# Kernel tuning notes

Measured on AMD Instinct MI355X. Metric: run time of the kernel, lower is better.

## Reference

```python
import jax, jax.numpy as jnp
import numpy as np

N_NODES = 100000
N_EDGES = 1000000
D = 128          # input_dim == hidden_dim (required: h = zeros_like(nh) accumulates src_nf)
OUT = 128
NUM_TYPES = 5


def setup_inputs() -> dict:
    key = jax.random.key(0)
    ks = jax.random.split(key, 7)
    nh = jax.random.normal(ks[0], (N_NODES, D), dtype=jnp.float32)
    edge_y = jax.random.randint(ks[1], (N_EDGES,), 0, NUM_TYPES, dtype=jnp.int64)
    edge_index = jax.random.randint(ks[2], (2, N_EDGES), 0, N_NODES, dtype=jnp.int64)
    # nn.Linear weights, scaled for numerical sanity
    W_nf = jax.random.normal(ks[3], (D, D), dtype=jnp.float32) * 0.08
    W_attn = jax.random.normal(ks[4], (1, 2 * D), dtype=jnp.float32) * 0.08
    W_out = jax.random.normal(ks[5], (OUT, 2 * D), dtype=jnp.float32) * 0.08
    b_out = jax.random.normal(ks[6], (OUT,), dtype=jnp.float32) * 0.01
    return {"nh": nh, "edge_y": edge_y, "edge_index": edge_index,
            "W_nf": W_nf, "W_attn": W_attn, "W_out": W_out, "b_out": b_out}


def reference(nh, edge_y, edge_index, W_nf, W_attn, W_out, b_out):
    n = nh.shape[0]
    src, dst = edge_index[0], edge_index[1]

    # nf_lin applied once per node, then gathered per edge (same math as
    # self.nf_lin(nh[src]) since Linear is per-row)
    nfl = nh @ W_nf.T                                  # [N, D]
    src_nf = nfl[src]                                  # [E, D]
    dst_nf = nfl[dst]                                  # [E, D]

    # attn(cat([src_nf, dst_nf])) == src_nf @ a_src + dst_nf @ a_dst
    a_src, a_dst = W_attn[0, :D], W_attn[0, D:]
    ef = src_nf @ a_src + dst_nf @ a_dst               # [E]
    ef = jnp.where(ef >= 0, ef, 0.2 * ef)              # LeakyReLU(0.2)

    # scatter_softmax per (edge_type, dst) group: the per-type loop with
    # scatter_softmax over dst is exactly a segment softmax over composite
    # segments seg = dst*5 + type; the summed per-type scatter_adds equal
    # one segment_sum over dst.
    seg = dst * NUM_TYPES + edge_y                     # [E]
    num_seg = n * NUM_TYPES
    m = jax.ops.segment_max(ef, seg, num_segments=num_seg)
    ex = jnp.exp(ef - m[seg])
    denom = jax.ops.segment_sum(ex, seg, num_segments=num_seg)
    alpha = ex / denom[seg]                            # [E]

    h = jax.ops.segment_sum(alpha[:, None] * src_nf, dst, num_segments=n)  # [N, D]

    nf = jnp.concatenate([nh, h], axis=-1) @ W_out.T + b_out
    return jax.nn.relu(nf)
```

## Files before the change

### kernel.cpp

```cpp
#include <hip/hip_runtime.h>

#define NTYPES 5
#define EPB 4096
#define BKSH 7
#define BKDST 128
#define SUBD 32
#define CAP 1024

typedef _Float16 half8 __attribute__((ext_vector_type(8)));
typedef _Float16 half4v __attribute__((ext_vector_type(4)));
typedef float float4v __attribute__((ext_vector_type(4)));

__device__ __forceinline__ void stage_f32(
    _Float16* lds, const float* __restrict__ g, int rows, int stride4, int off4,
    int grow0, int nmax, int t)
{
  const float4* g4 = (const float4*)g;
  for (int i = t; i < rows * 32; i += 256) {
    int row = i >> 5, q = i & 31;
    float4 v = make_float4(0.f, 0.f, 0.f, 0.f);
    int gr = grow0 + row;
    if (gr < nmax) v = g4[(size_t)gr * stride4 + off4 + q];
    half4v hv = { (_Float16)v.x, (_Float16)v.y, (_Float16)v.z, (_Float16)v.w };
    int byte = row * 256 + ((q * 8) ^ ((row & 7) << 4));
    *(half4v*)((char*)lds + byte) = hv;
  }
}

__device__ __forceinline__ half8 frag_ld(const _Float16* lds, int row, int khw) {
  int byte = row * 256 + ((khw * 2) ^ ((row & 7) << 4));
  return *(const half8*)((const char*)lds + byte);
}

__device__ __forceinline__ half8 cvt8(float4 v0, float4 v1) {
  half8 a;
  a[0] = (_Float16)v0.x; a[1] = (_Float16)v0.y; a[2] = (_Float16)v0.z; a[3] = (_Float16)v0.w;
  a[4] = (_Float16)v1.x; a[5] = (_Float16)v1.y; a[6] = (_Float16)v1.z; a[7] = (_Float16)v1.w;
  return a;
}

__global__ __launch_bounds__(256) void k_gemm0(
    const float* __restrict__ nh, const float* __restrict__ Wnf,
    const float* __restrict__ Wattn,
    float* __restrict__ s_src, float* __restrict__ s_dst,
    _Float16* __restrict__ nfl, _Float16* __restrict__ nh16, int n)
{
  __shared__ _Float16 wh[128 * 128];
  const int t = threadIdx.x, lane = t & 63, wv = t >> 6;
  const int r16 = lane & 15, g = lane >> 4;
  stage_f32(wh, Wnf, 128, 32, 0, 0, 1 << 30, t);
  float asrc[8], adst[8];
  #pragma unroll
  for (int nf = 0; nf < 8; ++nf) {
    asrc[nf] = Wattn[nf * 16 + r16];
    adst[nf] = Wattn[128 + nf * 16 + r16];
  }
  __syncthreads();
  const int nchunk = (n + 63) >> 6;
  for (int c = blockIdx.x; c < nchunk; c += gridDim.x) {
    const int base = c << 6;
    const int arow = base + wv * 16 + r16;
    const bool ok = arow < n;
    const float4* nh4 = (const float4*)(nh + (size_t)arow * 128);
    const float4 z = make_float4(0.f, 0.f, 0.f, 0.f);
    float4 av[8];
    #pragma unroll
    for (int s = 0; s < 4; ++s) {
      av[2 * s]     = ok ? nh4[s * 8 + g * 2]     : z;
      av[2 * s + 1] = ok ? nh4[s * 8 + g * 2 + 1] : z;
    }
    float4v acc[8];
    #pragma unroll
    for (int nf = 0; nf < 8; ++nf) acc[nf] = (float4v){0.f, 0.f, 0.f, 0.f};
    #pragma unroll
    for (int s = 0; s < 4; ++s) {
      half8 a = cvt8(av[2 * s], av[2 * s + 1]);
      if (ok) *(half8*)(nh16 + (size_t)arow * 128 + s * 32 + g * 8) = a;
      #pragma unroll
      for (int nf = 0; nf < 8; ++nf)
        acc[nf] = __builtin_amdgcn_mfma_f32_16x16x32_f16(a, frag_ld(wh, nf * 16 + r16, s * 32 + g * 8), acc[nf], 0, 0, 0);
    }
    #pragma unroll
    for (int rr = 0; rr < 4; ++rr) {
      int node = base + wv * 16 + g * 4 + rr;
      if (node >= n) continue;
      size_t ro = (size_t)node * 128;
      #pragma unroll
      for (int nf = 0; nf < 8; ++nf) nfl[ro + nf * 16 + r16] = (_Float16)acc[nf][rr];
    }
    float ss[4] = {0.f, 0.f, 0.f, 0.f}, sd[4] = {0.f, 0.f, 0.f, 0.f};
    #pragma unroll
    for (int nf = 0; nf < 8; ++nf)
      #pragma unroll
      for (int rr = 0; rr < 4; ++rr) {
        ss[rr] = fmaf(acc[nf][rr], asrc[nf], ss[rr]);
        sd[rr] = fmaf(acc[nf][rr], adst[nf], sd[rr]);
      }
    #pragma unroll
    for (int m = 1; m <= 8; m <<= 1)
      #pragma unroll
      for (int rr = 0; rr < 4; ++rr) {
        ss[rr] += __shfl_xor(ss[rr], m);
        sd[rr] += __shfl_xor(sd[rr], m);
      }
    if (r16 == 0) {
      #pragma unroll
      for (int rr = 0; rr < 4; ++rr) {
        int node = base + wv * 16 + g * 4 + rr;
        if (node < n) { s_src[node] = ss[rr]; s_dst[node] = sd[rr]; }
      }
    }
  }
}

__global__ __launch_bounds__(256) void k_hist(
    const int* __restrict__ dsts, int* __restrict__ cnt, int e, int nbk, int nblk)
{
  __shared__ int hist[1024];
  const int t = threadIdx.x, b = blockIdx.x;
  for (int k = t; k < nbk; k += 256) hist[k] = 0;
  __syncthreads();
  const int i0 = b * EPB;
  const int iend = min(i0 + EPB, e);
  for (int i = i0 + t; i < iend; i += 256)
    atomicAdd(&hist[dsts[i] >> BKSH], 1);
  __syncthreads();
  for (int k = t; k < nbk; k += 256) cnt[k * nblk + b] = hist[k];
}

__global__ __launch_bounds__(256) void k_scan1(
    const int* __restrict__ deg, int* __restrict__ base, int* __restrict__ bsum, int n)
{
  __shared__ int ws[4];
  int t = threadIdx.x;
  int g0 = blockIdx.x * 1024 + t * 4;
  int4 v = make_int4(0, 0, 0, 0);
  if (g0 + 3 < n) v = *(const int4*)(deg + g0);
  else {
    if (g0     < n) v.x = deg[g0];
    if (g0 + 1 < n) v.y = deg[g0 + 1];
    if (g0 + 2 < n) v.z = deg[g0 + 2];
    if (g0 + 3 < n) v.w = deg[g0 + 3];
  }
  int s = v.x + v.y + v.z + v.w;
  int inc = s;
  #pragma unroll
  for (int d = 1; d < 64; d <<= 1) {
    int o = __shfl_up(inc, d);
    if ((t & 63) >= d) inc += o;
  }
  int wid = t >> 6;
  if ((t & 63) == 63) ws[wid] = inc;
  __syncthreads();
  int woff = 0;
  for (int w = 0; w < wid; ++w) woff += ws[w];
  int exc = woff + inc - s;
  if (g0 + 3 < n) {
    *(int4*)(base + g0) = make_int4(exc, exc + v.x, exc + v.x + v.y, exc + v.x + v.y + v.z);
  } else {
    if (g0     < n) base[g0]     = exc;
    if (g0 + 1 < n) base[g0 + 1] = exc + v.x;
    if (g0 + 2 < n) base[g0 + 2] = exc + v.x + v.y;
  }
  if (t == 255) bsum[blockIdx.x] = woff + inc;
}

__global__ __launch_bounds__(256) void k_scan2(
    const int* __restrict__ bsum, int* __restrict__ boff, int nb)
{
  __shared__ int ws[4];
  int t = threadIdx.x;
  int x = t < nb ? bsum[t] : 0;
  int inc = x;
  #pragma unroll
  for (int d = 1; d < 64; d <<= 1) {
    int o = __shfl_up(inc, d);
    if ((t & 63) >= d) inc += o;
  }
  int wid = t >> 6;
  if ((t & 63) == 63) ws[wid] = inc;
  __syncthreads();
  int woff = 0;
  for (int w = 0; w < wid; ++w) woff += ws[w];
  if (t < nb) boff[t] = woff + inc - x;
}

__global__ __launch_bounds__(256) void k_scan3(
    int* __restrict__ base, const int* __restrict__ boff, int n)
{
  int i = blockIdx.x * 256 + threadIdx.x;
  if (i < n) base[i] += boff[i >> 10];
}

__global__ __launch_bounds__(256) void k_scatter2(
    const int* __restrict__ ei, const int* __restrict__ ey,
    const int* __restrict__ cnt_s, unsigned* __restrict__ rec,
    int e, int nbk, int nblk)
{
  __shared__ int cur[1024];
  const int t = threadIdx.x, b = blockIdx.x;
  for (int k = t; k < nbk; k += 256) cur[k] = cnt_s[k * nblk + b];
  __syncthreads();
  const int i0 = b * EPB;
  const int iend = min(i0 + EPB, e);
  for (int i = i0 + t; i < iend; i += 256) {
    int s = ei[i], d = ei[e + i], ty = ey[i];
    int pos = atomicAdd(&cur[d >> BKSH], 1);
    rec[pos] = (unsigned)s | ((unsigned)ty << 17) | ((unsigned)(d & (BKDST - 1)) << 20);
  }
}

__global__ __launch_bounds__(256) void k_agg2(
    const unsigned* __restrict__ rec, const int* __restrict__ cnt_s,
    const float* __restrict__ s_src, const float* __restrict__ s_dst,
    const _Float16* __restrict__ nfl, _Float16* __restrict__ h,
    int n, int e, int nbk, int nblk)
{
  __shared__ unsigned ord[CAP];
  __shared__ float efl[CAP];
  __shared__ int dcnt[SUBD];
  __shared__ int dbase[SUBD + 1];
  __shared__ float sdl[SUBD];
  const int t = threadIdx.x;
  const int sb = blockIdx.x;
  const int d0 = sb << 5;
  const int ndst = min(SUBD, n - d0);
  const int k = sb >> 2;
  const int sub = sb & 3;
  const int bs = cnt_s[k * nblk];
  const int be = (k + 1 < nbk) ? cnt_s[(k + 1) * nblk] : e;
  const int cnt = be - bs;
  if (t < SUBD) {
    dcnt[t] = 0;
    if (t < ndst) sdl[t] = s_dst[d0 + t];
  }
  __syncthreads();
  const int g = t >> 4, l = t & 15;

  for (int i = t; i < cnt; i += 256) {
    int dl = (rec[bs + i] >> 20) & 127;
    if ((dl >> 5) == sub) atomicAdd(&dcnt[dl & 31], 1);
  }
  __syncthreads();
  if (t < SUBD) {
    int v = dcnt[t];
    int inc = v;
    #pragma unroll
    for (int dd = 1; dd < SUBD; dd <<= 1) {
      int o = __shfl_up(inc, dd);
      if (t >= dd) inc += o;
    }
    dbase[t] = inc - v;
    dcnt[t]  = inc - v;
    if (t == SUBD - 1) dbase[SUBD] = inc;
  }
  __syncthreads();
  const int total = dbase[SUBD];

  if (total <= CAP) {
    for (int i = t; i < cnt; i += 256) {
      unsigned p = rec[bs + i];
      int dl = (p >> 20) & 127;
      if ((dl >> 5) == sub) {
        int pos = atomicAdd(&dcnt[dl & 31], 1);
        ord[pos] = p;
      }
    }
    __syncthreads();
    for (int i = t; i < total; i += 256) {
      unsigned p = ord[i];
      float ef = s_src[p & 0x1FFFF] + sdl[(p >> 20) & 31];
      efl[i] = ef >= 0.f ? ef : 0.2f * ef;
    }
    __syncthreads();
    for (int di = g; di < ndst; di += 16) {
      int s0 = dbase[di], deg = dbase[di + 1] - s0;
      float acc[8] = {0.f, 0.f, 0.f, 0.f, 0.f, 0.f, 0.f, 0.f};
      if (deg > 0) {
        float mx[NTYPES];
        #pragma unroll
        for (int tt = 0; tt < NTYPES; ++tt) mx[tt] = -1e30f;
        for (int j0 = 0; j0 < deg; j0 += 16) {
          int jj = j0 + l;
          bool ok = jj < deg;
          float ef = ok ? efl[s0 + jj] : -1e30f;
          int ty = ok ? (int)((ord[s0 + jj] >> 17) & 7) : 7;
          #pragma unroll
          for (int tt = 0; tt < NTYPES; ++tt) {
            float v = (ty == tt) ? ef : -1e30f;
            v = fmaxf(v, __shfl_xor(v, 1)); v = fmaxf(v, __shfl_xor(v, 2));
            v = fmaxf(v, __shfl_xor(v, 4)); v = fmaxf(v, __shfl_xor(v, 8));
            mx[tt] = fmaxf(mx[tt], v);
          }
        }
        float sm[NTYPES];
        #pragma unroll
        for (int tt = 0; tt < NTYPES; ++tt) sm[tt] = 0.f;
        for (int j0 = 0; j0 < deg; j0 += 16) {
          int jj = j0 + l;
          bool ok = jj < deg;
          int ty = ok ? (int)((ord[s0 + jj] >> 17) & 7) : 7;
          float ex = ok ? __expf(efl[s0 + jj] - mx[ty]) : 0.f;
          if (ok) efl[s0 + jj] = ex;
          #pragma unroll
          for (int tt = 0; tt < NTYPES; ++tt) {
            float v = (ty == tt) ? ex : 0.f;
            v += __shfl_xor(v, 1); v += __shfl_xor(v, 2);
            v += __shfl_xor(v, 4); v += __shfl_xor(v, 8);
            sm[tt] += v;
          }
        }
        float rsm[NTYPES];
        #pragma unroll
        for (int tt = 0; tt < NTYPES; ++tt) rsm[tt] = sm[tt] > 0.f ? 1.f / sm[tt] : 0.f;
        int j = 0;
        for (; j + 4 <= deg; j += 4) {
          unsigned p0 = ord[s0 + j],     p1 = ord[s0 + j + 1];
          unsigned p2 = ord[s0 + j + 2], p3 = ord[s0 + j + 3];
          float a0 = efl[s0 + j]     * rsm[(p0 >> 17) & 7];
          float a1 = efl[s0 + j + 1] * rsm[(p1 >> 17) & 7];
          float a2 = efl[s0 + j + 2] * rsm[(p2 >> 17) & 7];
          float a3 = efl[s0 + j + 3] * rsm[(p3 >> 17) & 7];
          half8 x0 = *(const half8*)(nfl + (size_t)(p0 & 0x1FFFF) * 128 + l * 8);
          half8 x1 = *(const half8*)(nfl + (size_t)(p1 & 0x1FFFF) * 128 + l * 8);
          half8 x2 = *(const half8*)(nfl + (size_t)(p2 & 0x1FFFF) * 128 + l * 8);
          half8 x3 = *(const half8*)(nfl + (size_t)(p3 & 0x1FFFF) * 128 + l * 8);
          #pragma unroll
          for (int kk = 0; kk < 8; ++kk) acc[kk] = fmaf(a0, (float)x0[kk], acc[kk]);
          #pragma unroll
          for (int kk = 0; kk < 8; ++kk) acc[kk] = fmaf(a1, (float)x1[kk], acc[kk]);
          #pragma unroll
          for (int kk = 0; kk < 8; ++kk) acc[kk] = fmaf(a2, (float)x2[kk], acc[kk]);
          #pragma unroll
          for (int kk = 0; kk < 8; ++kk) acc[kk] = fmaf(a3, (float)x3[kk], acc[kk]);
        }
        for (; j < deg; ++j) {
          unsigned p0 = ord[s0 + j];
          float a0 = efl[s0 + j] * rsm[(p0 >> 17) & 7];
          half8 x0 = *(const half8*)(nfl + (size_t)(p0 & 0x1FFFF) * 128 + l * 8);
          #pragma unroll
          for (int kk = 0; kk < 8; ++kk) acc[kk] = fmaf(a0, (float)x0[kk], acc[kk]);
        }
      }
      half8 hv;
      #pragma unroll
      for (int kk = 0; kk < 8; ++kk) hv[kk] = (_Float16)acc[kk];
      *(half8*)(h + (size_t)(d0 + di) * 128 + l * 8) = hv;
    }
  } else {
    const int gb = (t & 63) & 48;
    for (int di = g; di < ndst; di += 16) {
      const int want = sub * SUBD + di;
      float mx[NTYPES], sm[NTYPES];
      #pragma unroll
      for (int tt = 0; tt < NTYPES; ++tt) { mx[tt] = -1e30f; sm[tt] = 0.f; }
      for (int j0 = 0; j0 < cnt; j0 += 16) {
        int jj = j0 + l;
        unsigned p = (jj < cnt) ? rec[bs + jj] : 0xFFFFFFFFu;
        bool mine = (p != 0xFFFFFFFFu) && (int)((p >> 20) & 127) == want;
        float ef = -1e30f; int ty = 7;
        if (mine) {
          ef = s_src[p & 0x1FFFF] + sdl[di];
          ef = ef >= 0.f ? ef : 0.2f * ef;
          ty = (p >> 17) & 7;
        }
        #pragma unroll
        for (int tt = 0; tt < NTYPES; ++tt) {
          float v = (mine && ty == tt) ? ef : -1e30f;
          v = fmaxf(v, __shfl_xor(v, 1)); v = fmaxf(v, __shfl_xor(v, 2));
          v = fmaxf(v, __shfl_xor(v, 4)); v = fmaxf(v, __shfl_xor(v, 8));
          mx[tt] = fmaxf(mx[tt], v);
        }
      }
      for (int j0 = 0; j0 < cnt; j0 += 16) {
        int jj = j0 + l;
        unsigned p = (jj < cnt) ? rec[bs + jj] : 0xFFFFFFFFu;
        bool mine = (p != 0xFFFFFFFFu) && (int)((p >> 20) & 127) == want;
        float ex = 0.f; int ty = 7;
        if (mine) {
          float ef = s_src[p & 0x1FFFF] + sdl[di];
          ef = ef >= 0.f ? ef : 0.2f * ef;
          ty = (p >> 17) & 7;
          ex = __expf(ef - mx[ty]);
        }
        #pragma unroll
        for (int tt = 0; tt < NTYPES; ++tt) {
          float v = (ty == tt) ? ex : 0.f;
          v += __shfl_xor(v, 1); v += __shfl_xor(v, 2);
          v += __shfl_xor(v, 4); v += __shfl_xor(v, 8);
          sm[tt] += v;
        }
      }
      float rsm[NTYPES];
      #pragma unroll
      for (int tt = 0; tt < NTYPES; ++tt) rsm[tt] = sm[tt] > 0.f ? 1.f / sm[tt] : 0.f;
      float acc[8] = {0.f, 0.f, 0.f, 0.f, 0.f, 0.f, 0.f, 0.f};
      for (int j0 = 0; j0 < cnt; j0 += 16) {
        int jj = j0 + l;
        unsigned p = (jj < cnt) ? rec[bs + jj] : 0xFFFFFFFFu;
        bool mine = (p != 0xFFFFFFFFu) && (int)((p >> 20) & 127) == want;
        float al = 0.f;
        if (mine) {
          float ef = s_src[p & 0x1FFFF] + sdl[di];
          ef = ef >= 0.f ? ef : 0.2f * ef;
          int ty = (p >> 17) & 7;
          al = __expf(ef - mx[ty]) * rsm[ty];
        }
        unsigned pv = mine ? p : 0xFFFFFFFFu;
        for (int jj2 = 0; jj2 < 16; ++jj2) {
          unsigned pp = __shfl(pv, gb + jj2);
          float aa = __shfl(al, gb + jj2);
          if (pp != 0xFFFFFFFFu) {
            half8 x = *(const half8*)(nfl + (size_t)(pp & 0x1FFFF) * 128 + l * 8);
            #pragma unroll
            for (int kk = 0; kk < 8; ++kk) acc[kk] = fmaf(aa, (float)x[kk], acc[kk]);
          }
        }
      }
      half8 hv;
      #pragma unroll
      for (int kk = 0; kk < 8; ++kk) hv[kk] = (_Float16)acc[kk];
      *(half8*)(h + (size_t)(d0 + di) * 128 + l * 8) = hv;
    }
  }
}

__global__ __launch_bounds__(256) void k_gemmO(
    const _Float16* __restrict__ nh16, const _Float16* __restrict__ hbuf,
    const float* __restrict__ Wout, const float* __restrict__ bias,
    float* __restrict__ out, int n)
{
  __shared__ _Float16 w1[64 * 128], w2[64 * 128];
  const int t = threadIdx.x, lane = t & 63, wv = t >> 6;
  const int r16 = lane & 15, g = lane >> 4;
  const int jhalf = blockIdx.x & 1;
  stage_f32(w1, Wout, 64, 64, 0,  jhalf * 64, 1 << 30, t);
  stage_f32(w2, Wout, 64, 64, 32, jhalf * 64, 1 << 30, t);
  float bv[4];
  #pragma unroll
  for (int nf = 0; nf < 4; ++nf) bv[nf] = bias[jhalf * 64 + nf * 16 + r16];
  __syncthreads();
  const int nchunk = (n + 63) >> 6;
  const int gstride = gridDim.x >> 1;
  int c = blockIdx.x >> 1;
  half8 c1[4], c2[4];
  if (c < nchunk) {
    int arow = (c << 6) + wv * 16 + r16;
    bool ok = arow < n;
    #pragma unroll
    for (int s = 0; s < 4; ++s) {
      c1[s] = ok ? *(const half8*)(nh16 + (size_t)arow * 128 + s * 32 + g * 8) : (half8){};
      c2[s] = ok ? *(const half8*)(hbuf + (size_t)arow * 128 + s * 32 + g * 8) : (half8){};
    }
  }
  for (; c < nchunk; c += gstride) {
    const int base = c << 6;
    int cn = c + gstride;
    half8 n1[4] = {}, n2[4] = {};
    if (cn < nchunk) {
      int arow = (cn << 6) + wv * 16 + r16;
      bool ok = arow < n;
      #pragma unroll
      for (int s = 0; s < 4; ++s) {
        n1[s] = ok ? *(const half8*)(nh16 + (size_t)arow * 128 + s * 32 + g * 8) : (half8){};
        n2[s] = ok ? *(const half8*)(hbuf + (size_t)arow * 128 + s * 32 + g * 8) : (half8){};
      }
    }
    float4v acc[4];
    #pragma unroll
    for (int nf = 0; nf < 4; ++nf) acc[nf] = (float4v){0.f, 0.f, 0.f, 0.f};
    #pragma unroll
    for (int s = 0; s < 4; ++s) {
      #pragma unroll
      for (int nf = 0; nf < 4; ++nf) {
        acc[nf] = __builtin_amdgcn_mfma_f32_16x16x32_f16(c1[s], frag_ld(w1, nf * 16 + r16, s * 32 + g * 8), acc[nf], 0, 0, 0);
        acc[nf] = __builtin_amdgcn_mfma_f32_16x16x32_f16(c2[s], frag_ld(w2, nf * 16 + r16, s * 32 + g * 8), acc[nf], 0, 0, 0);
      }
    }
    #pragma unroll
    for (int rr = 0; rr < 4; ++rr) {
      int node = base + wv * 16 + g * 4 + rr;
      if (node >= n) continue;
      #pragma unroll
      for (int nf = 0; nf < 4; ++nf)
        out[(size_t)node * 128 + jhalf * 64 + nf * 16 + r16] = fmaxf(acc[nf][rr] + bv[nf], 0.f);
    }
    #pragma unroll
    for (int s = 0; s < 4; ++s) { c1[s] = n1[s]; c2[s] = n2[s]; }
  }
}

extern "C" void kernel_launch(void* const* d_in, const int* in_sizes, int n_in,
                              void* d_out, int out_size, void* d_ws, size_t ws_size,
                              hipStream_t stream) {
  const float* nh     = (const float*)d_in[0];
  const int*   edge_y = (const int*)d_in[1];
  const int*   ei     = (const int*)d_in[2];
  const float* W_nf   = (const float*)d_in[3];
  const float* W_attn = (const float*)d_in[4];
  const float* W_out  = (const float*)d_in[5];
  const float* b_out  = (const float*)d_in[6];
  float* out = (float*)d_out;
  const int n = in_sizes[0] / 128;
  const int e = in_sizes[1];
  const int nbk  = (n + BKDST - 1) >> BKSH;
  const int nblk = (e + EPB - 1) / EPB;
  const int ncnt = nbk * nblk;
  const int nb2  = (ncnt + 1023) / 1024;
  const int nsb  = (n + SUBD - 1) / SUBD;

  _Float16* nfl_h = (_Float16*)d_ws;
  _Float16* nh16  = nfl_h + (size_t)n * 128;
  _Float16* h_h   = nh16 + (size_t)n * 128;
  float* s_src = (float*)(h_h + (size_t)n * 128);
  float* s_dst = s_src + n;
  int*   cnt   = (int*)(s_dst + n);
  int*   bsum  = cnt + ncnt;
  int*   boff  = bsum + 256;
  unsigned* rec = (unsigned*)(boff + 256);

  k_gemm0<<<1280, 256, 0, stream>>>(nh, W_nf, W_attn, s_src, s_dst, nfl_h, nh16, n);
  k_hist<<<nblk, 256, 0, stream>>>(ei + e, cnt, e, nbk, nblk);
  k_scan1<<<nb2, 256, 0, stream>>>(cnt, cnt, bsum, ncnt);
  k_scan2<<<1, 256, 0, stream>>>(bsum, boff, nb2);
  k_scan3<<<(ncnt + 255) / 256, 256, 0, stream>>>(cnt, boff, ncnt);
  k_scatter2<<<nblk, 256, 0, stream>>>(ei, edge_y, cnt, rec, e, nbk, nblk);
  k_agg2<<<nsb, 256, 0, stream>>>(rec, cnt, s_src, s_dst, nfl_h, h_h, n, e, nbk, nblk);
  k_gemmO<<<1280, 256, 0, stream>>>(nh16, h_h, W_out, b_out, out, n);
}
```

Baseline: 165.4 us.

## Split attention scores into separate kernel and raise occupancy of GEMM kernels

```diff
diff --git a/kernel.cpp b/kernel.cpp
--- a/kernel.cpp
+++ b/kernel.cpp
@@ -39,22 +39,14 @@
   return a;
 }
 
-__global__ __launch_bounds__(256) void k_gemm0(
+__global__ __launch_bounds__(256, 5) void k_gemm0(
     const float* __restrict__ nh, const float* __restrict__ Wnf,
-    const float* __restrict__ Wattn,
-    float* __restrict__ s_src, float* __restrict__ s_dst,
     _Float16* __restrict__ nfl, _Float16* __restrict__ nh16, int n)
 {
   __shared__ _Float16 wh[128 * 128];
   const int t = threadIdx.x, lane = t & 63, wv = t >> 6;
   const int r16 = lane & 15, g = lane >> 4;
   stage_f32(wh, Wnf, 128, 32, 0, 0, 1 << 30, t);
-  float asrc[8], adst[8];
-  #pragma unroll
-  for (int nf = 0; nf < 8; ++nf) {
-    asrc[nf] = Wattn[nf * 16 + r16];
-    adst[nf] = Wattn[128 + nf * 16 + r16];
-  }
   __syncthreads();
   const int nchunk = (n + 63) >> 6;
   for (int c = blockIdx.x; c < nchunk; c += gridDim.x) {
@@ -88,29 +80,31 @@
       #pragma unroll
       for (int nf = 0; nf < 8; ++nf) nfl[ro + nf * 16 + r16] = (_Float16)acc[nf][rr];
     }
-    float ss[4] = {0.f, 0.f, 0.f, 0.f}, sd[4] = {0.f, 0.f, 0.f, 0.f};
-    #pragma unroll
-    for (int nf = 0; nf < 8; ++nf)
-      #pragma unroll
-      for (int rr = 0; rr < 4; ++rr) {
-        ss[rr] = fmaf(acc[nf][rr], asrc[nf], ss[rr]);
-        sd[rr] = fmaf(acc[nf][rr], adst[nf], sd[rr]);
-      }
-    #pragma unroll
-    for (int m = 1; m <= 8; m <<= 1)
-      #pragma unroll
-      for (int rr = 0; rr < 4; ++rr) {
-        ss[rr] += __shfl_xor(ss[rr], m);
-        sd[rr] += __shfl_xor(sd[rr], m);
-      }
-    if (r16 == 0) {
-      #pragma unroll
-      for (int rr = 0; rr < 4; ++rr) {
-        int node = base + wv * 16 + g * 4 + rr;
-        if (node < n) { s_src[node] = ss[rr]; s_dst[node] = sd[rr]; }
-      }
-    }
-  }
+  }
+}
+
+__global__ __launch_bounds__(256) void k_attn(
+    const _Float16* __restrict__ nfl, const float* __restrict__ Wattn,
+    float* __restrict__ s_src, float* __restrict__ s_dst, int n)
+{
+  const int grp = threadIdx.x >> 4, l = threadIdx.x & 15;
+  const int node = blockIdx.x * 16 + grp;
+  float4 wa0 = *(const float4*)(Wattn + l * 8);
+  float4 wa1 = *(const float4*)(Wattn + l * 8 + 4);
+  float4 wd0 = *(const float4*)(Wattn + 128 + l * 8);
+  float4 wd1 = *(const float4*)(Wattn + 128 + l * 8 + 4);
+  if (node >= n) return;
+  half8 x = *(const half8*)(nfl + (size_t)node * 128 + l * 8);
+  float ss = (float)x[0]*wa0.x + (float)x[1]*wa0.y + (float)x[2]*wa0.z + (float)x[3]*wa0.w
+           + (float)x[4]*wa1.x + (float)x[5]*wa1.y + (float)x[6]*wa1.z + (float)x[7]*wa1.w;
+  float sd = (float)x[0]*wd0.x + (float)x[1]*wd0.y + (float)x[2]*wd0.z + (float)x[3]*wd0.w
+           + (float)x[4]*wd1.x + (float)x[5]*wd1.y + (float)x[6]*wd1.z + (float)x[7]*wd1.w;
+  #pragma unroll
+  for (int m = 1; m <= 8; m <<= 1) {
+    ss += __shfl_xor(ss, m);
+    sd += __shfl_xor(sd, m);
+  }
+  if (l == 0) { s_src[node] = ss; s_dst[node] = sd; }
 }
 
 __global__ __launch_bounds__(256) void k_hist(
@@ -425,7 +419,7 @@
   }
 }
 
-__global__ __launch_bounds__(256) void k_gemmO(
+__global__ __launch_bounds__(256, 6) void k_gemmO(
     const _Float16* __restrict__ nh16, const _Float16* __restrict__ hbuf,
     const float* __restrict__ Wout, const float* __restrict__ bias,
     float* __restrict__ out, int n)
@@ -442,29 +436,14 @@
   __syncthreads();
   const int nchunk = (n + 63) >> 6;
   const int gstride = gridDim.x >> 1;
-  int c = blockIdx.x >> 1;
-  half8 c1[4], c2[4];
-  if (c < nchunk) {
-    int arow = (c << 6) + wv * 16 + r16;
-    bool ok = arow < n;
+  for (int c = blockIdx.x >> 1; c < nchunk; c += gstride) {
+    const int arow = (c << 6) + wv * 16 + r16;
+    const bool ok = arow < n;
+    half8 c1[4], c2[4];
     #pragma unroll
     for (int s = 0; s < 4; ++s) {
       c1[s] = ok ? *(const half8*)(nh16 + (size_t)arow * 128 + s * 32 + g * 8) : (half8){};
       c2[s] = ok ? *(const half8*)(hbuf + (size_t)arow * 128 + s * 32 + g * 8) : (half8){};
-    }
-  }
-  for (; c < nchunk; c += gstride) {
-    const int base = c << 6;
-    int cn = c + gstride;
-    half8 n1[4] = {}, n2[4] = {};
-    if (cn < nchunk) {
-      int arow = (cn << 6) + wv * 16 + r16;
-      bool ok = arow < n;
-      #pragma unroll
-      for (int s = 0; s < 4; ++s) {
-        n1[s] = ok ? *(const half8*)(nh16 + (size_t)arow * 128 + s * 32 + g * 8) : (half8){};
-        n2[s] = ok ? *(const half8*)(hbuf + (size_t)arow * 128 + s * 32 + g * 8) : (half8){};
-      }
     }
     float4v acc[4];
     #pragma unroll
@@ -479,14 +458,12 @@
     }
     #pragma unroll
     for (int rr = 0; rr < 4; ++rr) {
-      int node = base + wv * 16 + g * 4 + rr;
+      int node = (c << 6) + wv * 16 + g * 4 + rr;
       if (node >= n) continue;
       #pragma unroll
       for (int nf = 0; nf < 4; ++nf)
         out[(size_t)node * 128 + jhalf * 64 + nf * 16 + r16] = fmaxf(acc[nf][rr] + bv[nf], 0.f);
     }
-    #pragma unroll
-    for (int s = 0; s < 4; ++s) { c1[s] = n1[s]; c2[s] = n2[s]; }
   }
 }
 
@@ -519,7 +496,8 @@
   int*   boff  = bsum + 256;
   unsigned* rec = (unsigned*)(boff + 256);
 
-  k_gemm0<<<1280, 256, 0, stream>>>(nh, W_nf, W_attn, s_src, s_dst, nfl_h, nh16, n);
+  k_gemm0<<<1280, 256, 0, stream>>>(nh, W_nf, nfl_h, nh16, n);
+  k_attn<<<(n + 15) / 16, 256, 0, stream>>>(nfl_h, W_attn, s_src, s_dst, n);
   k_hist<<<nblk, 256, 0, stream>>>(ei + e, cnt, e, nbk, nblk);
   k_scan1<<<nb2, 256, 0, stream>>>(cnt, cnt, bsum, ncnt);
   k_scan2<<<1, 256, 0, stream>>>(bsum, boff, nb2);
```

New measurement: 239.7 us. +44.9%, slower.
